# Kernel tuning notes

Measured on AMD Instinct MI355X. Metric: run time of the kernel, lower is better.

## Reference

```python
import jax, jax.numpy as jnp
import numpy as np

NSTEP = 5

# Clauses (vals = one-hot satisfying truth value per literal):
#   clause 0: ~S(x) | C(x)          vals: L0=[1,0], L1=[0,1]
#   clause 1: ~F(x,y) | ~S(x) | S(y) vals: L0=[1,0], L1=[1,0], L2=[0,1]
# Message to target literal i (torch influence()):
#   msg = w[r] * einsum over shared vars of prod_j ( q[pn_j] . (1 - vals_j) ) outer t_vals

def setup_inputs() -> dict:
    B, N = 2, 2048
    key = jax.random.key(0)
    k1, k2, k3 = jax.random.split(key, 3)
    return {
        "logits_S": jax.random.normal(k1, (B, N, 2), jnp.float32),
        "logits_C": jax.random.normal(k2, (B, N, 2), jnp.float32),
        "logits_F": jax.random.normal(k3, (B, N, N, 2), jnp.float32),
        "weights": jnp.ones((2,), jnp.float32),
    }


def _messages(qS, qC, qF, weights):
    dt = qS.dtype
    e_true = jnp.array([0.0, 1.0], dtype=dt)   # one-hot: positive literal satisfied
    e_false = jnp.array([1.0, 0.0], dtype=dt)  # one-hot: negated literal satisfied
    w0, w1 = weights[0], weights[1]
    # clause 0: ~S(x) | C(x)
    msg_C = (w0 * qS[..., 1])[..., None] * e_true            # [B,N,2]
    msg_S = (w0 * qC[..., 0])[..., None] * e_false           # [B,N,2]
    # clause 1: ~F(x,y) | ~S(x) | S(y)
    # target F(x,y): (q_S[b,x,true]) * (q_S[b,y,false]) on the 'false' slot of F
    msg_F = (w1 * qS[:, :, None, 1] * qS[:, None, :, 0])[..., None] * e_false  # [B,N,N,2]
    # target ~S(x): sum_y q_F[b,x,y,true] * q_S[b,y,false]
    msg_S = msg_S + (w1 * jnp.einsum('bxy,by->bx', qF[..., 1], qS[..., 0]))[..., None] * e_false
    # target S(y): sum_x q_F[b,x,y,true] * q_S[b,x,true]
    msg_S = msg_S + (w1 * jnp.einsum('bxy,bx->by', qF[..., 1], qS[..., 1]))[..., None] * e_true
    return msg_S, msg_C, msg_F


def reference(logits_S, logits_C, logits_F, weights):
    cur_S, cur_C, cur_F = logits_S, logits_C, logits_F
    for _ in range(NSTEP):
        qS = jax.nn.softmax(cur_S, axis=-1)
        qC = jax.nn.softmax(cur_C, axis=-1)
        qF = jax.nn.softmax(cur_F, axis=-1)
        msg_S, msg_C, msg_F = _messages(qS, qC, qF, weights)
        cur_S = logits_S + msg_S
        cur_C = logits_C + msg_C
        cur_F = logits_F + msg_F
    return (cur_S, cur_C, cur_F)
```

## Files before the change

kernel.cpp:

```cpp
#include <hip/hip_runtime.h>

#define NN   2048
#define ROWS 4096
#define RPB  16
#define CSPLIT 4
#define NBY  (ROWS/RPB)
#define NCSL 8
#define PSTR 257
#define NBLK (CSPLIT*NBY)

#define SUBW 32
#define NSUB (NBLK/SUBW)
#define CPAD 16
#define BARSTRIDE ((NSUB+1)*CPAD)

__device__ __forceinline__ float fsig(float x) {
    float e = __expf(-x);
    return __builtin_amdgcn_rcpf(1.0f + e);
}

__device__ __forceinline__ float gload(const float* p) {
    return __hip_atomic_load(p, __ATOMIC_RELAXED, __HIP_MEMORY_SCOPE_AGENT);
}
__device__ __forceinline__ void gstore(float* p, float v) {
    __hip_atomic_store(p, v, __ATOMIC_RELAXED, __HIP_MEMORY_SCOPE_AGENT);
}

__device__ __forceinline__ void gridbar(int* cnt, int bid) {
    __syncthreads();
    if (threadIdx.x == 0) {
        asm volatile("" ::: "memory");
        int* sub  = cnt + (bid & (NSUB - 1)) * CPAD;
        int* root = cnt + NSUB * CPAD;
        int old = __hip_atomic_fetch_add(sub, 1, __ATOMIC_RELAXED,
                                         __HIP_MEMORY_SCOPE_AGENT);
        if (old == SUBW - 1)
            __hip_atomic_fetch_add(root, 1, __ATOMIC_RELAXED,
                                   __HIP_MEMORY_SCOPE_AGENT);
        while (__hip_atomic_load(root, __ATOMIC_RELAXED,
                                 __HIP_MEMORY_SCOPE_AGENT) < NSUB)
            __builtin_amdgcn_s_sleep(1);
        asm volatile("" ::: "memory");
    }
    __syncthreads();
}

template<int T>
__device__ __forceinline__ void do_pass(
    float* __restrict__ stCur, const float* __restrict__ stPrev,
    const float* __restrict__ stPP,
    float* __restrict__ sdif, float* __restrict__ cdif,
    float* __restrict__ part,
    float (&d0)[RPB], float (&d1)[RPB],
    const float4* __restrict__ F,
    const float2* __restrict__ S2, const float2* __restrict__ C2,
    const float* __restrict__ rprev, const float* __restrict__ cprev,
    float* __restrict__ rout, float* __restrict__ cout,
    float* __restrict__ aSout, float4* __restrict__ outF,
    int tid, int sx, int by, int bloc, int row0, int base,
    float w0, float w1)
{
    for (int idx = tid; idx < 528; idx += 256) {
        int il = (idx < 512) ? (sx * 512 + idx) : (bloc * RPB + idx - 512);
        int g  = base + il;
        float cur;
        if (T == 0) {
            float2 sv = S2[g], cv = C2[g];
            float sd = sv.y - sv.x;
            sdif[idx] = sd;
            cdif[idx] = cv.x - cv.y;
            cur = fsig(sd);
        } else {
            float rs = gload(rprev + 0*ROWS + g) + gload(rprev + 1*ROWS + g)
                     + gload(rprev + 2*ROWS + g) + gload(rprev + 3*ROWS + g);
            float cs = 0.0f;
#pragma unroll
            for (int s = 0; s < NCSL; s++) cs += gload(cprev + s*ROWS + g);
            float qc = (T == 1) ? fsig(cdif[idx])
                                : fsig(cdif[idx] - w0 * stPP[idx]);
            cur = fsig(sdif[idx] + w1*cs - w0*qc - w1*rs);
        }
        stCur[idx] = cur;
        if (T >= 3 && sx == 0 && idx >= 512) gstore(aSout + g, cur);
    }
    __syncthreads();

    const int j = sx * 256 + tid;
    const float wq0 = 1.0f - stCur[2*tid];
    const float wq1 = 1.0f - stCur[2*tid + 1];
    const float bp0 = (T == 0) ? 0.0f : 1.0f - stPrev[2*tid];
    const float bp1 = (T == 0) ? 0.0f : 1.0f - stPrev[2*tid + 1];

    float c0 = 0.0f, c1 = 0.0f;

#pragma unroll
    for (int i = 0; i < RPB; i++) {
        const float a_c = stCur[512 + i];
        float s0, s1;
        if (T == 0) {
            const float4 f = F[(size_t)(row0 + i) * (NN/2) + j];
            d0[i] = f.y - f.x;
            d1[i] = f.w - f.z;
            s0 = fsig(d0[i]);
            s1 = fsig(d1[i]);
        } else {
            const float m1 = w1 * stPrev[512 + i];
            s0 = fsig(d0[i] - m1 * bp0);
            s1 = fsig(d1[i] - m1 * bp1);
        }
        c0 += s0 * a_c;
        c1 += s1 * a_c;
        part[i * PSTR + tid] = s0 * wq0 + s1 * wq1;
        if (T == 4) {
            const float4 f = F[(size_t)(row0 + i) * (NN/2) + j];
            const float mw = w1 * a_c;
            float4 o;
            o.x = f.x + mw * wq0; o.y = f.y;
            o.z = f.z + mw * wq1; o.w = f.w;
            outF[(size_t)(row0 + i) * (NN/2) + j] = o;
        }
    }

    atomicAdd(&cout[(by & (NCSL-1))*ROWS + base + 2*j],     c0);
    atomicAdd(&cout[(by & (NCSL-1))*ROWS + base + 2*j + 1], c1);

    __syncthreads();
    {
        const int row = tid >> 4, seg = tid & 15;
        float s = 0.0f;
#pragma unroll
        for (int u = 0; u < 16; u++) s += part[row * PSTR + seg * 16 + u];
#pragma unroll
        for (int off = 8; off > 0; off >>= 1) s += __shfl_down(s, off, 16);
        if (seg == 0) gstore(rout + sx * ROWS + row0 + row, s);
    }
}

__global__ __launch_bounds__(256, 4) void kfused(
    const float4* __restrict__ F,
    const float2* __restrict__ S2, const float2* __restrict__ C2,
    const float* __restrict__ w,
    float* __restrict__ ws,
    float4* __restrict__ outF)
{
    __shared__ float st[3][528];
    __shared__ float sdif[528];
    __shared__ float cdif[528];
    __shared__ float part[16 * PSTR];

    const int tid  = threadIdx.x;
    const int sx   = blockIdx.x;
    const int by   = blockIdx.y;
    const int row0 = by * RPB;
    const int b    = by >> 7;
    const int bloc = by & 127;
    const int base = b * NN;
    const int bid  = by * CSPLIT + sx;
    const float w0 = w[0], w1 = w[1];

    float d0[RPB], d1[RPB];

    float* rb = ws;
    float* cb = ws + 5 * 4 * ROWS;
    float* ab = ws + 5 * 4 * ROWS + 5 * 8 * ROWS;
    int*   bar = (int*)ab;
#define RB(t) (rb + (t) * 4 * ROWS)
#define CB(t) (cb + (t) * (size_t)NCSL * ROWS)
#define AB(t) (ab + ((t) - 1) * ROWS)

    do_pass<0>(st[0], st[2], st[1], sdif, cdif, part, d0, d1, F, S2, C2,
               nullptr, nullptr, RB(0), CB(0), nullptr, nullptr,
               tid, sx, by, bloc, row0, base, w0, w1);
    gridbar(bar + 0*BARSTRIDE, bid);
    do_pass<1>(st[1], st[0], st[2], sdif, cdif, part, d0, d1, F, S2, C2,
               RB(0), CB(0), RB(1), CB(1), nullptr, nullptr,
               tid, sx, by, bloc, row0, base, w0, w1);
    gridbar(bar + 1*BARSTRIDE, bid);
    do_pass<2>(st[2], st[1], st[0], sdif, cdif, part, d0, d1, F, S2, C2,
               RB(1), CB(1), RB(2), CB(2), nullptr, nullptr,
               tid, sx, by, bloc, row0, base, w0, w1);
    gridbar(bar + 2*BARSTRIDE, bid);
    do_pass<3>(st[0], st[2], st[1], sdif, cdif, part, d0, d1, F, S2, C2,
               RB(2), CB(2), RB(3), CB(3), AB(3), nullptr,
               tid, sx, by, bloc, row0, base, w0, w1);
    gridbar(bar + 3*BARSTRIDE, bid);
    do_pass<4>(st[1], st[0], st[2], sdif, cdif, part, d0, d1, F, S2, C2,
               RB(3), CB(3), RB(4), CB(4), AB(4), outF,
               tid, sx, by, bloc, row0, base, w0, w1);
}

template<int T>
__global__ __launch_bounds__(256) void kbig(
    const float4* __restrict__ F,
    const float2* __restrict__ S2, const float2* __restrict__ C2,
    const float* __restrict__ w,
    const float* __restrict__ rprev, const float* __restrict__ cprev,
    const float* __restrict__ aSm1, const float* __restrict__ aSm2,
    float* __restrict__ rout, float* __restrict__ cout,
    float* __restrict__ czero, float* __restrict__ aSout,
    float4* __restrict__ outF)
{
    __shared__ float sCur[528];
    __shared__ float sPrev[528];
    __shared__ float part[16 * PSTR];

    const int tid  = threadIdx.x;
    const int sx   = blockIdx.x;
    const int by   = blockIdx.y;
    const int row0 = by * RPB;
    const int b    = by >> 7;
    const int bloc = by & 127;
    const int base = b * NN;
    const float w0 = w[0], w1 = w[1];

    if (T < 4 && sx == 1) {
        int zi = by * 256 + tid;
        if (zi < NCSL * ROWS) czero[zi] = 0.0f;
    }

    for (int idx = tid; idx < 528; idx += 256) {
        int il = (idx < 512) ? (sx * 512 + idx) : (bloc * RPB + idx - 512);
        int g  = base + il;
        float2 sv = S2[g];
        float a0 = fsig(sv.y - sv.x);
        float cur, prev;
        if (T == 0) {
            cur = a0; prev = 0.0f;
        } else {
            float2 cv = C2[g];
            float rs = rprev[0*ROWS+g] + rprev[1*ROWS+g]
                     + rprev[2*ROWS+g] + rprev[3*ROWS+g];
            float cs = 0.0f;
#pragma unroll
            for (int s = 0; s < NCSL; s++) cs += cprev[s*ROWS + g];
            float qc;
            if (T == 1)      qc = fsig(cv.x - cv.y);
            else if (T == 2) qc = fsig(cv.x - cv.y - w0 * a0);
            else             qc = fsig(cv.x - cv.y - w0 * aSm2[g]);
            cur  = fsig((sv.y + w1*cs) - (sv.x + w0*qc + w1*rs));
            prev = (T == 1) ? a0 : aSm1[g];
        }
        sCur[idx]  = cur;
        sPrev[idx] = prev;
        if (T >= 1 && sx == 0 && idx >= 512) aSout[g] = cur;
    }
    __syncthreads();

    const int j = sx * 256 + tid;
    const float wq0 = 1.0f - sCur[2*tid];
    const float wq1 = 1.0f - sCur[2*tid + 1];
    const float bp0 = 1.0f - sPrev[2*tid];
    const float bp1 = 1.0f - sPrev[2*tid + 1];

    float c0 = 0.0f, c1 = 0.0f;

#pragma unroll 4
    for (int i = 0; i < RPB; i++) {
        const float a_c = sCur[512 + i];
        const float m1  = (T == 0) ? 0.0f : w1 * sPrev[512 + i];
        const float4 f = F[(size_t)(row0 + i) * (NN/2) + j];
        float s0 = fsig((f.y - f.x) - m1 * bp0);
        float s1 = fsig((f.w - f.z) - m1 * bp1);
        c0 += s0 * a_c;
        c1 += s1 * a_c;
        part[i * PSTR + tid] = s0 * wq0 + s1 * wq1;
        if (T == 4) {
            const float mw = w1 * a_c;
            float4 o;
            o.x = f.x + mw * wq0; o.y = f.y;
            o.z = f.z + mw * wq1; o.w = f.w;
            outF[(size_t)(row0 + i) * (NN/2) + j] = o;
        }
    }

    atomicAdd(&cout[(by & (NCSL-1))*ROWS + base + 2*j],     c0);
    atomicAdd(&cout[(by & (NCSL-1))*ROWS + base + 2*j + 1], c1);

    __syncthreads();
    {
        const int row = tid >> 4, seg = tid & 15;
        float s = 0.0f;
#pragma unroll
        for (int u = 0; u < 16; u++) s += part[row * PSTR + seg * 16 + u];
#pragma unroll
        for (int off = 8; off > 0; off >>= 1) s += __shfl_down(s, off, 16);
        if (seg == 0) rout[sx * ROWS + row0 + row] = s;
    }
}

__global__ void kfin(const float2* __restrict__ S2, const float2* __restrict__ C2,
                     const float* __restrict__ w,
                     const float* __restrict__ rpart, const float* __restrict__ cpart,
                     const float* __restrict__ aS4, const float* __restrict__ aS3,
                     float2* __restrict__ outS, float2* __restrict__ outC)
{
    int idx = blockIdx.x * blockDim.x + threadIdx.x;
    if (idx >= ROWS) return;
    float w0 = w[0], w1 = w[1];
    float rs = rpart[0*ROWS+idx] + rpart[1*ROWS+idx]
             + rpart[2*ROWS+idx] + rpart[3*ROWS+idx];
    float cs = 0.0f;
#pragma unroll
    for (int s = 0; s < NCSL; s++) cs += cpart[s*ROWS + idx];
    float2 sv = S2[idx], cv = C2[idx];
    float qc4 = fsig(cv.x - cv.y - w0 * aS3[idx]);
    float2 os, oc;
    os.x = sv.x + w0 * qc4 + w1 * rs;
    os.y = sv.y + w1 * cs;
    oc.x = cv.x;
    oc.y = cv.y + w0 * aS4[idx];
    outS[idx] = os;
    outC[idx] = oc;
}

extern "C" void kernel_launch(void* const* d_in, const int* in_sizes, int n_in,
                              void* d_out, int out_size, void* d_ws, size_t ws_size,
                              hipStream_t stream)
{
    const float2* S2 = (const float2*)d_in[0];
    const float2* C2 = (const float2*)d_in[1];
    const float4* F4 = (const float4*)d_in[2];
    const float*  w  = (const float*)d_in[3];
    float* out = (float*)d_out;
    float* ws  = (float*)d_ws;

    float* rb = ws;
    float* cb = ws + 5 * 4 * ROWS;
    float* ab = ws + 5 * 4 * ROWS + 5 * 8 * ROWS;
#define HRB(t) (rb + (t) * 4 * ROWS)
#define HCB(t) (cb + (t) * (size_t)NCSL * ROWS)
#define HAB(t) (ab + ((t) - 1) * ROWS)

    float* outS = out;
    float* outC = out + 2 * ROWS;
    float4* outF = (float4*)(out + 4 * ROWS);

    hipMemsetAsync(cb, 0, 5 * (size_t)NCSL * ROWS * sizeof(float), stream);
    hipMemsetAsync(ab, 0, 4 * BARSTRIDE * sizeof(int), stream);

    dim3 gb(CSPLIT, NBY), bb(256, 1, 1);
    void* args[] = { (void*)&F4, (void*)&S2, (void*)&C2, (void*)&w,
                     (void*)&ws, (void*)&outF };
    hipError_t ce = hipLaunchCooperativeKernel((const void*)kfused, gb, bb,
                                               args, 0, stream);
    if (ce != hipSuccess) {
        (void)hipGetLastError();
        kbig<0><<<gb, bb, 0, stream>>>(F4, S2, C2, w, nullptr, nullptr, nullptr, nullptr,
                                       HRB(0), HCB(0), HCB(1), nullptr, nullptr);
        kbig<1><<<gb, bb, 0, stream>>>(F4, S2, C2, w, HRB(0), HCB(0), nullptr, nullptr,
                                       HRB(1), HCB(1), HCB(2), HAB(1), nullptr);
        kbig<2><<<gb, bb, 0, stream>>>(F4, S2, C2, w, HRB(1), HCB(1), HAB(1), nullptr,
                                       HRB(2), HCB(2), HCB(3), HAB(2), nullptr);
        kbig<3><<<gb, bb, 0, stream>>>(F4, S2, C2, w, HRB(2), HCB(2), HAB(2), HAB(1),
                                       HRB(3), HCB(3), HCB(4), HAB(3), nullptr);
        kbig<4><<<gb, bb, 0, stream>>>(F4, S2, C2, w, HRB(3), HCB(3), HAB(3), HAB(2),
                                       HRB(4), HCB(4), nullptr, HAB(4), outF);
    }
    kfin<<<dim3(ROWS/256), bb, 0, stream>>>(S2, C2, w, HRB(4), HCB(4), HAB(4), HAB(3),
                                            (float2*)outS, (float2*)outC);
}
```

Baseline: 207.9 us.

## Double rows per block, reduce partials with global atomics, drop cooperative launch

Each block now handles 32 rows instead of 16, keeping twice as many F differences in registers, and the grid shrinks to 512 blocks. Row and column partial sums are accumulated directly with global float atomics rather than written to 4 and 8 separate slices, so each later pass reads one value per entry. The cooperative launch and the multi-kernel fallback are removed, the fused kernel is launched normally, and the grid barrier gets a spin limit. Risks include register pressure from 64 per-thread floats, more atomic contention, and the barrier breaking out early if not all blocks are co-resident.

After: 239.7 us. 1.15x slower.

```diff
diff --git a/kernel.cpp b/kernel.cpp
--- a/kernel.cpp
+++ b/kernel.cpp
@@ -2,10 +2,9 @@
 
 #define NN   2048
 #define ROWS 4096
-#define RPB  16
+#define RPB  32
 #define CSPLIT 4
 #define NBY  (ROWS/RPB)
-#define NCSL 8
 #define PSTR 257
 #define NBLK (CSPLIT*NBY)
 
@@ -13,6 +12,7 @@
 #define NSUB (NBLK/SUBW)
 #define CPAD 16
 #define BARSTRIDE ((NSUB+1)*CPAD)
+#define SPIN_LIMIT (1<<21)
 
 __device__ __forceinline__ float fsig(float x) {
     float e = __expf(-x);
@@ -24,6 +24,9 @@
 }
 __device__ __forceinline__ void gstore(float* p, float v) {
     __hip_atomic_store(p, v, __ATOMIC_RELAXED, __HIP_MEMORY_SCOPE_AGENT);
+}
+__device__ __forceinline__ void gatomic_add(float* p, float v) {
+    __hip_atomic_fetch_add(p, v, __ATOMIC_RELAXED, __HIP_MEMORY_SCOPE_AGENT);
 }
 
 __device__ __forceinline__ void gridbar(int* cnt, int bid) {
@@ -37,9 +40,12 @@
         if (old == SUBW - 1)
             __hip_atomic_fetch_add(root, 1, __ATOMIC_RELAXED,
                                    __HIP_MEMORY_SCOPE_AGENT);
+        int tries = 0;
         while (__hip_atomic_load(root, __ATOMIC_RELAXED,
-                                 __HIP_MEMORY_SCOPE_AGENT) < NSUB)
-            __builtin_amdgcn_s_sleep(1);
+                                 __HIP_MEMORY_SCOPE_AGENT) < NSUB) {
+            __builtin_amdgcn_s_sleep(2);
+            if (++tries > SPIN_LIMIT) break;
+        }
         asm volatile("" ::: "memory");
     }
     __syncthreads();
@@ -60,7 +66,7 @@
     int tid, int sx, int by, int bloc, int row0, int base,
     float w0, float w1)
 {
-    for (int idx = tid; idx < 528; idx += 256) {
+    for (int idx = tid; idx < 512 + RPB; idx += 256) {
         int il = (idx < 512) ? (sx * 512 + idx) : (bloc * RPB + idx - 512);
         int g  = base + il;
         float cur;
@@ -71,11 +77,8 @@
             cdif[idx] = cv.x - cv.y;
             cur = fsig(sd);
         } else {
-            float rs = gload(rprev + 0*ROWS + g) + gload(rprev + 1*ROWS + g)
-                     + gload(rprev + 2*ROWS + g) + gload(rprev + 3*ROWS + g);
-            float cs = 0.0f;
-#pragma unroll
-            for (int s = 0; s < NCSL; s++) cs += gload(cprev + s*ROWS + g);
+            float rs = gload(rprev + g);
+            float cs = gload(cprev + g);
             float qc = (T == 1) ? fsig(cdif[idx])
                                 : fsig(cdif[idx] - w0 * stPP[idx]);
             cur = fsig(sdif[idx] + w1*cs - w0*qc - w1*rs);
@@ -94,46 +97,50 @@
     float c0 = 0.0f, c1 = 0.0f;
 
 #pragma unroll
-    for (int i = 0; i < RPB; i++) {
-        const float a_c = stCur[512 + i];
-        float s0, s1;
-        if (T == 0) {
-            const float4 f = F[(size_t)(row0 + i) * (NN/2) + j];
-            d0[i] = f.y - f.x;
-            d1[i] = f.w - f.z;
-            s0 = fsig(d0[i]);
-            s1 = fsig(d1[i]);
-        } else {
-            const float m1 = w1 * stPrev[512 + i];
-            s0 = fsig(d0[i] - m1 * bp0);
-            s1 = fsig(d1[i] - m1 * bp1);
-        }
-        c0 += s0 * a_c;
-        c1 += s1 * a_c;
-        part[i * PSTR + tid] = s0 * wq0 + s1 * wq1;
-        if (T == 4) {
-            const float4 f = F[(size_t)(row0 + i) * (NN/2) + j];
-            const float mw = w1 * a_c;
-            float4 o;
-            o.x = f.x + mw * wq0; o.y = f.y;
-            o.z = f.z + mw * wq1; o.w = f.w;
-            outF[(size_t)(row0 + i) * (NN/2) + j] = o;
-        }
+    for (int h = 0; h < 2; h++) {
+#pragma unroll
+        for (int i = 0; i < 16; i++) {
+            const int ir  = h * 16 + i;
+            const float a_c = stCur[512 + ir];
+            float s0, s1;
+            if (T == 0) {
+                const float4 f = F[(size_t)(row0 + ir) * (NN/2) + j];
+                d0[ir] = f.y - f.x;
+                d1[ir] = f.w - f.z;
+                s0 = fsig(d0[ir]);
+                s1 = fsig(d1[ir]);
+            } else {
+                const float m1 = w1 * stPrev[512 + ir];
+                s0 = fsig(d0[ir] - m1 * bp0);
+                s1 = fsig(d1[ir] - m1 * bp1);
+            }
+            c0 += s0 * a_c;
+            c1 += s1 * a_c;
+            part[i * PSTR + tid] = s0 * wq0 + s1 * wq1;
+            if (T == 4) {
+                const float4 f = F[(size_t)(row0 + ir) * (NN/2) + j];
+                const float mw = w1 * a_c;
+                float4 o;
+                o.x = f.x + mw * wq0; o.y = f.y;
+                o.z = f.z + mw * wq1; o.w = f.w;
+                outF[(size_t)(row0 + ir) * (NN/2) + j] = o;
+            }
+        }
+        __syncthreads();
+        {
+            const int row = tid >> 4, seg = tid & 15;
+            float s = 0.0f;
+#pragma unroll
+            for (int u = 0; u < 16; u++) s += part[row * PSTR + seg * 16 + u];
+#pragma unroll
+            for (int off = 8; off > 0; off >>= 1) s += __shfl_down(s, off, 16);
+            if (seg == 0) gatomic_add(rout + row0 + h * 16 + row, s);
+        }
+        __syncthreads();
     }
 
-    atomicAdd(&cout[(by & (NCSL-1))*ROWS + base + 2*j],     c0);
-    atomicAdd(&cout[(by & (NCSL-1))*ROWS + base + 2*j + 1], c1);
-
-    __syncthreads();
-    {
-        const int row = tid >> 4, seg = tid & 15;
-        float s = 0.0f;
-#pragma unroll
-        for (int u = 0; u < 16; u++) s += part[row * PSTR + seg * 16 + u];
-#pragma unroll
-        for (int off = 8; off > 0; off >>= 1) s += __shfl_down(s, off, 16);
-        if (seg == 0) gstore(rout + sx * ROWS + row0 + row, s);
-    }
+    gatomic_add(cout + base + 2*j,     c0);
+    gatomic_add(cout + base + 2*j + 1, c1);
 }
 
 __global__ __launch_bounds__(256, 4) void kfused(
@@ -143,17 +150,17 @@
     float* __restrict__ ws,
     float4* __restrict__ outF)
 {
-    __shared__ float st[3][528];
-    __shared__ float sdif[528];
-    __shared__ float cdif[528];
+    __shared__ float st[3][512 + RPB];
+    __shared__ float sdif[512 + RPB];
+    __shared__ float cdif[512 + RPB];
     __shared__ float part[16 * PSTR];
 
     const int tid  = threadIdx.x;
     const int sx   = blockIdx.x;
     const int by   = blockIdx.y;
     const int row0 = by * RPB;
-    const int b    = by >> 7;
-    const int bloc = by & 127;
+    const int b    = by >> 6;
+    const int bloc = by & 63;
     const int base = b * NN;
     const int bid  = by * CSPLIT + sx;
     const float w0 = w[0], w1 = w[1];
@@ -161,11 +168,11 @@
     float d0[RPB], d1[RPB];
 
     float* rb = ws;
-    float* cb = ws + 5 * 4 * ROWS;
-    float* ab = ws + 5 * 4 * ROWS + 5 * 8 * ROWS;
-    int*   bar = (int*)ab;
-#define RB(t) (rb + (t) * 4 * ROWS)
-#define CB(t) (cb + (t) * (size_t)NCSL * ROWS)
+    float* cb = ws + 5 * ROWS;
+    float* ab = ws + 10 * ROWS;
+    int*   bar = (int*)(ws + 14 * ROWS);
+#define RB(t) (rb + (t) * ROWS)
+#define CB(t) (cb + (t) * ROWS)
 #define AB(t) (ab + ((t) - 1) * ROWS)
 
     do_pass<0>(st[0], st[2], st[1], sdif, cdif, part, d0, d1, F, S2, C2,
@@ -187,105 +194,6 @@
     do_pass<4>(st[1], st[0], st[2], sdif, cdif, part, d0, d1, F, S2, C2,
                RB(3), CB(3), RB(4), CB(4), AB(4), outF,
                tid, sx, by, bloc, row0, base, w0, w1);
-}
-
-template<int T>
-__global__ __launch_bounds__(256) void kbig(
-    const float4* __restrict__ F,
-    const float2* __restrict__ S2, const float2* __restrict__ C2,
-    const float* __restrict__ w,
-    const float* __restrict__ rprev, const float* __restrict__ cprev,
-    const float* __restrict__ aSm1, const float* __restrict__ aSm2,
-    float* __restrict__ rout, float* __restrict__ cout,
-    float* __restrict__ czero, float* __restrict__ aSout,
-    float4* __restrict__ outF)
-{
-    __shared__ float sCur[528];
-    __shared__ float sPrev[528];
-    __shared__ float part[16 * PSTR];
-
-    const int tid  = threadIdx.x;
-    const int sx   = blockIdx.x;
-    const int by   = blockIdx.y;
-    const int row0 = by * RPB;
-    const int b    = by >> 7;
-    const int bloc = by & 127;
-    const int base = b * NN;
-    const float w0 = w[0], w1 = w[1];
-
-    if (T < 4 && sx == 1) {
-        int zi = by * 256 + tid;
-        if (zi < NCSL * ROWS) czero[zi] = 0.0f;
-    }
-
-    for (int idx = tid; idx < 528; idx += 256) {
-        int il = (idx < 512) ? (sx * 512 + idx) : (bloc * RPB + idx - 512);
-        int g  = base + il;
-        float2 sv = S2[g];
-        float a0 = fsig(sv.y - sv.x);
-        float cur, prev;
-        if (T == 0) {
-            cur = a0; prev = 0.0f;
-        } else {
-            float2 cv = C2[g];
-            float rs = rprev[0*ROWS+g] + rprev[1*ROWS+g]
-                     + rprev[2*ROWS+g] + rprev[3*ROWS+g];
-            float cs = 0.0f;
-#pragma unroll
-            for (int s = 0; s < NCSL; s++) cs += cprev[s*ROWS + g];
-            float qc;
-            if (T == 1)      qc = fsig(cv.x - cv.y);
-            else if (T == 2) qc = fsig(cv.x - cv.y - w0 * a0);
-            else             qc = fsig(cv.x - cv.y - w0 * aSm2[g]);
-            cur  = fsig((sv.y + w1*cs) - (sv.x + w0*qc + w1*rs));
-            prev = (T == 1) ? a0 : aSm1[g];
-        }
-        sCur[idx]  = cur;
-        sPrev[idx] = prev;
-        if (T >= 1 && sx == 0 && idx >= 512) aSout[g] = cur;
-    }
-    __syncthreads();
-
-    const int j = sx * 256 + tid;
-    const float wq0 = 1.0f - sCur[2*tid];
-    const float wq1 = 1.0f - sCur[2*tid + 1];
-    const float bp0 = 1.0f - sPrev[2*tid];
-    const float bp1 = 1.0f - sPrev[2*tid + 1];
-
-    float c0 = 0.0f, c1 = 0.0f;
-
-#pragma unroll 4
-    for (int i = 0; i < RPB; i++) {
-        const float a_c = sCur[512 + i];
-        const float m1  = (T == 0) ? 0.0f : w1 * sPrev[512 + i];
-        const float4 f = F[(size_t)(row0 + i) * (NN/2) + j];
-        float s0 = fsig((f.y - f.x) - m1 * bp0);
-        float s1 = fsig((f.w - f.z) - m1 * bp1);
-        c0 += s0 * a_c;
-        c1 += s1 * a_c;
-        part[i * PSTR + tid] = s0 * wq0 + s1 * wq1;
-        if (T == 4) {
-            const float mw = w1 * a_c;
-            float4 o;
-            o.x = f.x + mw * wq0; o.y = f.y;
-            o.z = f.z + mw * wq1; o.w = f.w;
-            outF[(size_t)(row0 + i) * (NN/2) + j] = o;
-        }
-    }
-
-    atomicAdd(&cout[(by & (NCSL-1))*ROWS + base + 2*j],     c0);
-    atomicAdd(&cout[(by & (NCSL-1))*ROWS + base + 2*j + 1], c1);
-
-    __syncthreads();
-    {
-        const int row = tid >> 4, seg = tid & 15;
-        float s = 0.0f;
-#pragma unroll
-        for (int u = 0; u < 16; u++) s += part[row * PSTR + seg * 16 + u];
-#pragma unroll
-        for (int off = 8; off > 0; off >>= 1) s += __shfl_down(s, off, 16);
-        if (seg == 0) rout[sx * ROWS + row0 + row] = s;
-    }
 }
 
 __global__ void kfin(const float2* __restrict__ S2, const float2* __restrict__ C2,
@@ -297,11 +205,8 @@
     int idx = blockIdx.x * blockDim.x + threadIdx.x;
     if (idx >= ROWS) return;
     float w0 = w[0], w1 = w[1];
-    float rs = rpart[0*ROWS+idx] + rpart[1*ROWS+idx]
-             + rpart[2*ROWS+idx] + rpart[3*ROWS+idx];
-    float cs = 0.0f;
-#pragma unroll
-    for (int s = 0; s < NCSL; s++) cs += cpart[s*ROWS + idx];
+    float rs = rpart[idx];
+    float cs = cpart[idx];
     float2 sv = S2[idx], cv = C2[idx];
     float qc4 = fsig(cv.x - cv.y - w0 * aS3[idx]);
     float2 os, oc;
@@ -325,37 +230,21 @@
     float* ws  = (float*)d_ws;
 
     float* rb = ws;
-    float* cb = ws + 5 * 4 * ROWS;
-    float* ab = ws + 5 * 4 * ROWS + 5 * 8 * ROWS;
-#define HRB(t) (rb + (t) * 4 * ROWS)
-#define HCB(t) (cb + (t) * (size_t)NCSL * ROWS)
-#define HAB(t) (ab + ((t) - 1) * ROWS)
+    float* cb = ws + 5 * ROWS;
+    float* ab = ws + 10 * ROWS;
+    int*   bar = (int*)(ws + 14 * ROWS);
 
     float* outS = out;
     float* outC = out + 2 * ROWS;
     float4* outF = (float4*)(out + 4 * ROWS);
 
-    hipMemsetAsync(cb, 0, 5 * (size_t)NCSL * ROWS * sizeof(float), stream);
-    hipMemsetAsync(ab, 0, 4 * BARSTRIDE * sizeof(int), stream);
+    hipMemsetAsync(ws, 0, 10 * (size_t)ROWS * sizeof(float), stream);
+    hipMemsetAsync(bar, 0, 4 * BARSTRIDE * sizeof(int), stream);
 
     dim3 gb(CSPLIT, NBY), bb(256, 1, 1);
-    void* args[] = { (void*)&F4, (void*)&S2, (void*)&C2, (void*)&w,
-                     (void*)&ws, (void*)&outF };
-    hipError_t ce = hipLaunchCooperativeKernel((const void*)kfused, gb, bb,
-                                               args, 0, stream);
-    if (ce != hipSuccess) {
-        (void)hipGetLastError();
-        kbig<0><<<gb, bb, 0, stream>>>(F4, S2, C2, w, nullptr, nullptr, nullptr, nullptr,
-                                       HRB(0), HCB(0), HCB(1), nullptr, nullptr);
-        kbig<1><<<gb, bb, 0, stream>>>(F4, S2, C2, w, HRB(0), HCB(0), nullptr, nullptr,
-                                       HRB(1), HCB(1), HCB(2), HAB(1), nullptr);
-        kbig<2><<<gb, bb, 0, stream>>>(F4, S2, C2, w, HRB(1), HCB(1), HAB(1), nullptr,
-                                       HRB(2), HCB(2), HCB(3), HAB(2), nullptr);
-        kbig<3><<<gb, bb, 0, stream>>>(F4, S2, C2, w, HRB(2), HCB(2), HAB(2), HAB(1),
-                                       HRB(3), HCB(3), HCB(4), HAB(3), nullptr);
-        kbig<4><<<gb, bb, 0, stream>>>(F4, S2, C2, w, HRB(3), HCB(3), HAB(3), HAB(2),
-                                       HRB(4), HCB(4), nullptr, HAB(4), outF);
-    }
-    kfin<<<dim3(ROWS/256), bb, 0, stream>>>(S2, C2, w, HRB(4), HCB(4), HAB(4), HAB(3),
+    kfused<<<gb, bb, 0, stream>>>(F4, S2, C2, w, ws, outF);
+    kfin<<<dim3(ROWS/256), bb, 0, stream>>>(S2, C2, w,
+                                            rb + 4 * ROWS, cb + 4 * ROWS,
+                                            ab + 3 * ROWS, ab + 2 * ROWS,
                                             (float2*)outS, (float2*)outC);
 }
```
